# Kernel optimization log

Measured on AMD Instinct MI355X. Metric: run time of the kernel, lower is better.

Reference implementation:

```python
import jax, jax.numpy as jnp
import numpy as np

D_MODEL = 1024
NUM_HEAD = 16
HIDDEN = D_MODEL // NUM_HEAD  # 64, also d_att
T = float(np.sqrt(HIDDEN))
L = 2048
BS = 2


def setup_inputs() -> dict:
    key = jax.random.key(0)
    ks = jax.random.split(key, 6)
    s = 1.0 / np.sqrt(D_MODEL)
    return {
        "Q": jax.random.normal(ks[0], (L, BS, D_MODEL), jnp.float32),
        "K": jax.random.normal(ks[1], (L, BS, D_MODEL), jnp.float32),
        "V": jax.random.normal(ks[2], (L, BS, D_MODEL), jnp.float32),
        "WQ": jax.random.normal(ks[3], (D_MODEL, D_MODEL), jnp.float32) * s,
        "bQ": jnp.zeros((D_MODEL,), jnp.float32),
        "WK": jax.random.normal(ks[4], (D_MODEL, D_MODEL), jnp.float32) * s,
        "bK": jnp.zeros((D_MODEL,), jnp.float32),
        "Wp": jax.random.normal(ks[5], (D_MODEL, 2 * D_MODEL), jnp.float32) * s,
        "bp": jnp.zeros((D_MODEL,), jnp.float32),
    }


def reference(Q, K, V, WQ, bQ, WK, bK, Wp, bp):
    # inputs are sequence-first: [L, bs, d_model]
    Lq, bs, _ = Q.shape
    Qp = (Q @ WQ.T + bQ) / T
    Kp = K @ WK.T + bK
    # [L, bs, d_model] -> [bs, h, L, d]
    q = Qp.reshape(Lq, bs, NUM_HEAD, HIDDEN).transpose(1, 2, 0, 3)
    k = Kp.reshape(-1, bs, NUM_HEAD, HIDDEN).transpose(1, 2, 0, 3)
    v = V.reshape(-1, bs, NUM_HEAD, HIDDEN).transpose(1, 2, 0, 3)
    scores = jnp.einsum('bhqd,bhkd->bhqk', q, k)
    # use_dis: 2*QK - ||K||^2 per key
    scores = 2.0 * scores - jnp.sum(k * k, axis=-1)[:, :, None, :]
    attn = jax.nn.softmax(scores, axis=-1)
    out = jnp.einsum('bhqk,bhkd->bhqd', attn, v)
    out = out.transpose(2, 0, 1, 3).reshape(Lq, bs, D_MODEL)
    combined = jnp.concatenate([out, V], axis=-1)
    proj = combined @ Wp.T + bp
    return proj, attn
```

## Files before the change

### kernel.cpp

```cpp
#include <hip/hip_runtime.h>
#include <hip/hip_bf16.h>

#define L_SEQ 2048
#define BSZ 2
#define DMODEL 1024
#define NHEAD 16
#define NROWS 4096

typedef __attribute__((ext_vector_type(8))) short bf16x8;
typedef __attribute__((ext_vector_type(4))) float f32x4;
typedef unsigned short u16;
typedef unsigned int u32;

__device__ __forceinline__ u16 f2bf(float x) {
  union { __hip_bfloat16 h; u16 u; } cv;
  cv.h = __float2bfloat16(x);
  return cv.u;
}

__device__ __forceinline__ void async16(void* lds, const void* g) {
  __builtin_amdgcn_global_load_lds(
      (const __attribute__((address_space(1))) void*)g,
      (__attribute__((address_space(3))) void*)lds, 16, 0, 0);
}

__global__ __launch_bounds__(256) void cvt_kernel(const float* __restrict__ s,
                                                  u16* __restrict__ d, int n) {
  int i = (blockIdx.x * 256 + threadIdx.x) * 4;
  if (i >= n) return;
  float4 v = *(const float4*)(s + i);
  ushort4 o;
  o.x = f2bf(v.x); o.y = f2bf(v.y); o.z = f2bf(v.z); o.w = f2bf(v.w);
  *(ushort4*)(d + i) = o;
}

__global__ __launch_bounds__(256) void cvtV_kernel(const float* __restrict__ s,
                                                   u16* __restrict__ comb) {
  int i = (blockIdx.x * 256 + threadIdx.x) * 4;
  if (i >= NROWS * DMODEL) return;
  int r = i >> 10, c = i & 1023;
  float4 v = *(const float4*)(s + i);
  ushort4 o;
  o.x = f2bf(v.x); o.y = f2bf(v.y); o.z = f2bf(v.z); o.w = f2bf(v.w);
  *(ushort4*)(comb + (size_t)r * 2048 + 1024 + c) = o;
}

__global__ __launch_bounds__(256) void gemm_bt(
    const u16* __restrict__ A, const u16* __restrict__ B,
    const float* __restrict__ bias, float scale,
    u16* __restrict__ Cb, float* __restrict__ Cf, float* __restrict__ ksq_out,
    int M, int N, int K) {
  __shared__ u16 As[128 * 64];
  __shared__ u16 Bs[128 * 64];
  const int tid = threadIdx.x;
  const int w = tid >> 6, lane = tid & 63;
  const int quad = lane >> 4, m16 = lane & 15;
  const int wr = w >> 1, wc = w & 1;
  const int m0 = blockIdx.y * 128, n0 = blockIdx.x * 128;
  f32x4 acc[4][4] = {};

  for (int kt = 0; kt < K; kt += 64) {
    __syncthreads();
#pragma unroll
    for (int j = 0; j < 4; ++j) {
      int chunk = (w * 4 + j) * 64 + lane;
      int row = chunk >> 3, kc = chunk & 7;
      async16(As + (size_t)(w * 4 + j) * 512,
              A + (size_t)(m0 + row) * K + kt + kc * 8);
      async16(Bs + (size_t)(w * 4 + j) * 512,
              B + (size_t)(n0 + row) * K + kt + kc * 8);
    }
    __syncthreads();
#pragma unroll
    for (int kk = 0; kk < 2; ++kk) {
      bf16x8 af[4], bfr[4];
#pragma unroll
      for (int i = 0; i < 4; ++i)
        af[i] = *(const bf16x8*)(As + (wr * 64 + i * 16 + m16) * 64 + kk * 32 + quad * 8);
#pragma unroll
      for (int j = 0; j < 4; ++j)
        bfr[j] = *(const bf16x8*)(Bs + (wc * 64 + j * 16 + m16) * 64 + kk * 32 + quad * 8);
#pragma unroll
      for (int i = 0; i < 4; ++i)
#pragma unroll
        for (int j = 0; j < 4; ++j)
          acc[i][j] = __builtin_amdgcn_mfma_f32_16x16x32_bf16(af[i], bfr[j], acc[i][j], 0, 0, 0);
    }
  }

#pragma unroll
  for (int i = 0; i < 4; ++i) {
    int R0 = m0 + wr * 64 + i * 16 + quad * 4;
    float ksq_part[4] = {0.f, 0.f, 0.f, 0.f};
#pragma unroll
    for (int j = 0; j < 4; ++j) {
      int C = n0 + wc * 64 + j * 16 + m16;
      float bv = bias ? bias[C] : 0.0f;
#pragma unroll
      for (int r = 0; r < 4; ++r) {
        float v = (acc[i][j][r] + bv) * scale;
        size_t idx = (size_t)(R0 + r) * N + C;
        if (Cb) Cb[idx] = f2bf(v);
        if (Cf) Cf[idx] = v;
        if (ksq_out) ksq_part[r] += v * v;
      }
    }
    if (ksq_out) {
#pragma unroll
      for (int r = 0; r < 4; ++r) {
        float t = ksq_part[r];
        t += __shfl_xor(t, 1); t += __shfl_xor(t, 2);
        t += __shfl_xor(t, 4); t += __shfl_xor(t, 8);
        if (m16 == 0) {
          int R = R0 + r;
          int bb = R & 1, l = R >> 1;
          int h = (n0 + wc * 64) >> 6;
          ksq_out[(size_t)(bb * NHEAD + h) * L_SEQ + l] = t;
        }
      }
    }
  }
}

__global__ __launch_bounds__(256) void attn_kernel(
    const u16* __restrict__ qp, const u16* __restrict__ kp,
    const float* __restrict__ ksqg, const u16* __restrict__ comb_v,
    u16* __restrict__ comb_o, float* __restrict__ attn_out) {
  __shared__ u16 Qs[64 * 64];
  __shared__ u16 Ks[64 * 64];
  __shared__ u16 Vst[64 * 64];
  __shared__ u16 Ps[4 * 16 * 64];
  __shared__ float ksq_s[64];
  const int tid = threadIdx.x;
  const int w = tid >> 6, lane = tid & 63;
  const int quad = lane >> 4, m16 = lane & 15;
  const int qt = blockIdx.x, bh = blockIdx.y;
  const int b = bh >> 4, h = bh & 15;
  const int q0 = qt * 64;
  const int rsw = (m16 & 7) << 3;

#pragma unroll
  for (int j = 0; j < 2; ++j) {
    int chunk = (w * 2 + j) * 64 + lane;
    int row = chunk >> 3, kc = chunk & 7;
    int kcs = kc ^ (row & 7);
    async16(Qs + (size_t)(w * 2 + j) * 512,
            qp + (size_t)((q0 + row) * 2 + b) * 1024 + h * 64 + kcs * 8);
  }
  __syncthreads();
  bf16x8 aq0 = *(const bf16x8*)(Qs + (w * 16 + m16) * 64 + ((quad * 8) ^ rsw));
  bf16x8 aq1 = *(const bf16x8*)(Qs + (w * 16 + m16) * 64 + ((32 + quad * 8) ^ rsw));

  float lsum[4] = {0.f, 0.f, 0.f, 0.f};
  for (int kt = 0; kt < 32; ++kt) {
    __syncthreads();
#pragma unroll
    for (int j = 0; j < 2; ++j) {
      int chunk = (w * 2 + j) * 64 + lane;
      int row = chunk >> 3, kc = chunk & 7;
      int kcs = kc ^ (row & 7);
      async16(Ks + (size_t)(w * 2 + j) * 512,
              kp + (size_t)((kt * 64 + row) * 2 + b) * 1024 + h * 64 + kcs * 8);
    }
    if (tid < 64) ksq_s[tid] = ksqg[(size_t)bh * L_SEQ + kt * 64 + tid];
    __syncthreads();
#pragma unroll
    for (int j = 0; j < 4; ++j) {
      const u16* kr = Ks + (j * 16 + m16) * 64;
      bf16x8 bk0 = *(const bf16x8*)(kr + ((quad * 8) ^ rsw));
      bf16x8 bk1 = *(const bf16x8*)(kr + ((32 + quad * 8) ^ rsw));
      f32x4 s4 = {0.f, 0.f, 0.f, 0.f};
      __builtin_amdgcn_s_setprio(1);
      s4 = __builtin_amdgcn_mfma_f32_16x16x32_bf16(aq0, bk0, s4, 0, 0, 0);
      s4 = __builtin_amdgcn_mfma_f32_16x16x32_bf16(aq1, bk1, s4, 0, 0, 0);
      __builtin_amdgcn_s_setprio(0);
      float kq = ksq_s[j * 16 + m16];
#pragma unroll
      for (int r = 0; r < 4; ++r) lsum[r] += __expf(s4[r] - kq);
    }
  }
#pragma unroll
  for (int r = 0; r < 4; ++r) {
    float t = lsum[r];
    t += __shfl_xor(t, 1); t += __shfl_xor(t, 2);
    t += __shfl_xor(t, 4); t += __shfl_xor(t, 8);
    lsum[r] = 1.0f / t;
  }

  f32x4 o[4] = {};
  for (int kt = 0; kt < 32; ++kt) {
    __syncthreads();
#pragma unroll
    for (int j = 0; j < 2; ++j) {
      int chunk = (w * 2 + j) * 64 + lane;
      int row = chunk >> 3, kc = chunk & 7;
      int kcs = kc ^ (row & 7);
      async16(Ks + (size_t)(w * 2 + j) * 512,
              kp + (size_t)((kt * 64 + row) * 2 + b) * 1024 + h * 64 + kcs * 8);
    }
#pragma unroll
    for (int it = 0; it < 2; ++it) {
      int chunk = it * 256 + tid;
      int key = chunk >> 3, dc = chunk & 7;
      const u16* gp = comb_v + (size_t)((kt * 64 + key) * 2 + b) * 2048 + 1024 + h * 64 + dc * 8;
      uint4 u = *(const uint4*)gp;
      u32 parts[4] = {u.x, u.y, u.z, u.w};
#pragma unroll
      for (int q2 = 0; q2 < 4; ++q2) {
        int dA = dc * 8 + q2 * 2;
        int dB = dA + 1;
        int kxA = key ^ (((dc ^ (dA & 7)) & 7) << 3);
        int kxB = key ^ (((dc ^ (dB & 7)) & 7) << 3);
        Vst[dA * 64 + kxA] = (u16)(parts[q2] & 0xffffu);
        Vst[dB * 64 + kxB] = (u16)(parts[q2] >> 16);
      }
    }
    if (tid < 64) ksq_s[tid] = ksqg[(size_t)bh * L_SEQ + kt * 64 + tid];
    __syncthreads();
#pragma unroll
    for (int j = 0; j < 4; ++j) {
      const u16* kr = Ks + (j * 16 + m16) * 64;
      bf16x8 bk0 = *(const bf16x8*)(kr + ((quad * 8) ^ rsw));
      bf16x8 bk1 = *(const bf16x8*)(kr + ((32 + quad * 8) ^ rsw));
      f32x4 s4 = {0.f, 0.f, 0.f, 0.f};
      __builtin_amdgcn_s_setprio(1);
      s4 = __builtin_amdgcn_mfma_f32_16x16x32_bf16(aq0, bk0, s4, 0, 0, 0);
      s4 = __builtin_amdgcn_mfma_f32_16x16x32_bf16(aq1, bk1, s4, 0, 0, 0);
      __builtin_amdgcn_s_setprio(0);
      float kq = ksq_s[j * 16 + m16];
      size_t abase = ((size_t)bh * L_SEQ + q0 + w * 16 + quad * 4) * L_SEQ + kt * 64 + j * 16 + m16;
#pragma unroll
      for (int r = 0; r < 4; ++r) {
        float p = __expf(s4[r] - kq) * lsum[r];
        attn_out[abase + (size_t)r * L_SEQ] = p;
        int qrow = quad * 4 + r;
        int col = j * 16 + m16;
        Ps[w * 1024 + qrow * 64 + (col ^ ((qrow & 7) << 3))] = f2bf(p);
      }
    }
    __syncthreads();
#pragma unroll
    for (int kk = 0; kk < 2; ++kk) {
      bf16x8 pa = *(const bf16x8*)(Ps + w * 1024 + m16 * 64 +
                                   (((kk * 32 + quad * 8)) ^ rsw));
      __builtin_amdgcn_s_setprio(1);
#pragma unroll
      for (int j2 = 0; j2 < 4; ++j2) {
        int d = j2 * 16 + m16;
        int vx = (((d >> 3) ^ (d & 7)) & 7) << 3;
        bf16x8 bv = *(const bf16x8*)(Vst + d * 64 + ((kk * 32 + quad * 8) ^ vx));
        o[j2] = __builtin_amdgcn_mfma_f32_16x16x32_bf16(pa, bv, o[j2], 0, 0, 0);
      }
      __builtin_amdgcn_s_setprio(0);
    }
  }
#pragma unroll
  for (int j2 = 0; j2 < 4; ++j2) {
#pragma unroll
    for (int r = 0; r < 4; ++r) {
      int qrow = q0 + w * 16 + quad * 4 + r;
      comb_o[(size_t)(qrow * 2 + b) * 2048 + h * 64 + j2 * 16 + m16] = f2bf(o[j2][r]);
    }
  }
}

extern "C" void kernel_launch(void* const* d_in, const int* in_sizes, int n_in,
                              void* d_out, int out_size, void* d_ws, size_t ws_size,
                              hipStream_t stream) {
  const float* Q  = (const float*)d_in[0];
  const float* K  = (const float*)d_in[1];
  const float* V  = (const float*)d_in[2];
  const float* WQ = (const float*)d_in[3];
  const float* bQ = (const float*)d_in[4];
  const float* WK = (const float*)d_in[5];
  const float* bK = (const float*)d_in[6];
  const float* Wp = (const float*)d_in[7];
  const float* bp = (const float*)d_in[8];
  float* proj_out = (float*)d_out;
  float* attn_out = proj_out + (size_t)NROWS * DMODEL;

  char* ws = (char*)d_ws;
  const size_t MB = 1u << 20;
  u16* Qb   = (u16*)(ws + 0 * MB);
  u16* Kb   = (u16*)(ws + 8 * MB);
  u16* WQb  = (u16*)(ws + 16 * MB);
  u16* WKb  = (u16*)(ws + 18 * MB);
  u16* Wpb  = (u16*)(ws + 20 * MB);
  u16* qpb  = (u16*)(ws + 24 * MB);
  u16* kpb  = (u16*)(ws + 32 * MB);
  u16* comb = (u16*)(ws + 40 * MB);
  float* ksqb = (float*)(ws + 56 * MB);

  cvt_kernel<<<4096, 256, 0, stream>>>(Q, Qb, NROWS * DMODEL);
  cvt_kernel<<<4096, 256, 0, stream>>>(K, Kb, NROWS * DMODEL);
  cvt_kernel<<<1024, 256, 0, stream>>>(WQ, WQb, DMODEL * DMODEL);
  cvt_kernel<<<1024, 256, 0, stream>>>(WK, WKb, DMODEL * DMODEL);
  cvt_kernel<<<2048, 256, 0, stream>>>(Wp, Wpb, DMODEL * 2 * DMODEL);
  cvtV_kernel<<<4096, 256, 0, stream>>>(V, comb);

  gemm_bt<<<dim3(8, 32), 256, 0, stream>>>(Qb, WQb, bQ, 0.25f, qpb, nullptr, nullptr,
                                           NROWS, DMODEL, DMODEL);
  gemm_bt<<<dim3(8, 32), 256, 0, stream>>>(Kb, WKb, bK, 1.0f, kpb, nullptr, ksqb,
                                           NROWS, DMODEL, DMODEL);
  attn_kernel<<<dim3(32, 32), 256, 0, stream>>>(qpb, kpb, ksqb, comb, comb, attn_out);
  gemm_bt<<<dim3(8, 32), 256, 0, stream>>>(comb, Wpb, bp, 1.0f, nullptr, proj_out, nullptr,
                                           NROWS, DMODEL, 2 * DMODEL);
}
```

Measured before the change: 834.5 us.

## Double-buffer K/V tiles in attention with pre-transposed V and larger query tiles

Rewrites the attention kernel to process 128 queries per block with 32 rows per wave. K and V tiles are double-buffered in dynamic shared memory via async global-to-LDS loads, and the next tile's key norms are prefetched into registers. A new kernel pre-transposes V into a bf16 head-major layout, which removes the per-iteration scalar LDS transpose scatter. Blocks are remapped for locality and an occupancy hint is added. The cost is 80KB of LDS per block and an extra transpose kernel reusing the Qb buffer.

```diff
diff --git a/kernel.cpp b/kernel.cpp
--- a/kernel.cpp
+++ b/kernel.cpp
@@ -43,6 +43,32 @@
   ushort4 o;
   o.x = f2bf(v.x); o.y = f2bf(v.y); o.z = f2bf(v.z); o.w = f2bf(v.w);
   *(ushort4*)(comb + (size_t)r * 2048 + 1024 + c) = o;
+}
+
+__global__ __launch_bounds__(256) void transposeV_kernel(const float* __restrict__ V,
+                                                         u16* __restrict__ vt) {
+  __shared__ u16 T[64][80];
+  const int tid = threadIdx.x;
+  const int k0 = blockIdx.x * 64;
+  const int bh = blockIdx.y;
+  const int b = bh >> 4, h = bh & 15;
+#pragma unroll
+  for (int u = 0; u < 4; ++u) {
+    int key = u * 16 + (tid >> 4);
+    int d4 = (tid & 15) * 4;
+    float4 v = *(const float4*)(V + ((size_t)(k0 + key) * 2 + b) * 1024 + h * 64 + d4);
+    T[d4 + 0][key] = f2bf(v.x);
+    T[d4 + 1][key] = f2bf(v.y);
+    T[d4 + 2][key] = f2bf(v.z);
+    T[d4 + 3][key] = f2bf(v.w);
+  }
+  __syncthreads();
+  int d = tid >> 2, kq = (tid & 3) * 16;
+  uint4 lo = *(const uint4*)&T[d][kq];
+  uint4 hi = *(const uint4*)&T[d][kq + 8];
+  u16* dst = vt + ((size_t)bh * 64 + d) * 2048 + k0 + kq;
+  *(uint4*)dst = lo;
+  *(uint4*)(dst + 8) = hi;
 }
 
 __global__ __launch_bounds__(256) void gemm_bt(
@@ -122,146 +148,226 @@
   }
 }
 
-__global__ __launch_bounds__(256) void attn_kernel(
+__global__ __launch_bounds__(256, 2) void attn_kernel(
     const u16* __restrict__ qp, const u16* __restrict__ kp,
-    const float* __restrict__ ksqg, const u16* __restrict__ comb_v,
+    const float* __restrict__ ksqg, const u16* __restrict__ vt,
     u16* __restrict__ comb_o, float* __restrict__ attn_out) {
-  __shared__ u16 Qs[64 * 64];
-  __shared__ u16 Ks[64 * 64];
-  __shared__ u16 Vst[64 * 64];
-  __shared__ u16 Ps[4 * 16 * 64];
-  __shared__ float ksq_s[64];
+  extern __shared__ u16 smem[];
+
   const int tid = threadIdx.x;
   const int w = tid >> 6, lane = tid & 63;
   const int quad = lane >> 4, m16 = lane & 15;
-  const int qt = blockIdx.x, bh = blockIdx.y;
+  const int id = blockIdx.x;
+  const int wg = (id & 7) * 64 + (id >> 3);
+  const int bh = wg >> 4, qt = wg & 15;
   const int b = bh >> 4, h = bh & 15;
-  const int q0 = qt * 64;
-  const int rsw = (m16 & 7) << 3;
-
-#pragma unroll
-  for (int j = 0; j < 2; ++j) {
-    int chunk = (w * 2 + j) * 64 + lane;
-    int row = chunk >> 3, kc = chunk & 7;
-    int kcs = kc ^ (row & 7);
-    async16(Qs + (size_t)(w * 2 + j) * 512,
-            qp + (size_t)((q0 + row) * 2 + b) * 1024 + h * 64 + kcs * 8);
-  }
+  const int q0 = qt * 128;
+  u16* psw = smem + 32768 + w * 2048;
+
+#pragma unroll
+  for (int u = 0; u < 4; ++u) {
+    int base = u * 256 + w * 64;
+    int chunk = base + lane;
+    int kpr = chunk >> 4, g = chunk & 15;
+    int gs = g ^ (kpr & 15);
+    int qrow = q0 + kpr * 2 + (gs >> 3);
+    int dg = gs & 7;
+    async16(smem + 8192 + base * 8, qp + ((size_t)(qrow * 2 + b)) * 1024 + h * 64 + dg * 8);
+  }
+#pragma unroll
+  for (int u = 0; u < 4; ++u) {
+    int base = u * 256 + w * 64;
+    int chunk = base + lane;
+    int kpr = chunk >> 4, g = chunk & 15;
+    int gs = g ^ (kpr & 15);
+    int key = kpr * 2 + (gs >> 3);
+    int dg = gs & 7;
+    async16(smem + base * 8, kp + ((size_t)(key * 2 + b)) * 1024 + h * 64 + dg * 8);
+  }
+  float kqc[8], kqn[8];
+#pragma unroll
+  for (int j = 0; j < 8; ++j) kqc[j] = ksqg[(size_t)bh * L_SEQ + j * 16 + m16];
   __syncthreads();
-  bf16x8 aq0 = *(const bf16x8*)(Qs + (w * 16 + m16) * 64 + ((quad * 8) ^ rsw));
-  bf16x8 aq1 = *(const bf16x8*)(Qs + (w * 16 + m16) * 64 + ((32 + quad * 8) ^ rsw));
-
-  float lsum[4] = {0.f, 0.f, 0.f, 0.f};
-  for (int kt = 0; kt < 32; ++kt) {
+
+  bf16x8 aq[2][2];
+#pragma unroll
+  for (int qs = 0; qs < 2; ++qs)
+#pragma unroll
+    for (int hf = 0; hf < 2; ++hf) {
+      int rowloc = w * 32 + qs * 16 + m16;
+      int kpr = rowloc >> 1, hi2 = rowloc & 1;
+      int gs = hi2 * 8 + hf * 4 + quad;
+      int g = gs ^ (kpr & 15);
+      aq[qs][hf] = *(const bf16x8*)(smem + 8192 + kpr * 128 + g * 8);
+    }
+  __syncthreads();
+
+  float ls[2][4] = {};
+  for (int t = 0; t < 16; ++t) {
+    const int cur = t & 1;
+    const u16* kb = smem + (cur ? 8192 : 0);
+    u16* kbn = smem + (cur ? 0 : 8192);
+    if (t < 15) {
+#pragma unroll
+      for (int u = 0; u < 4; ++u) {
+        int base = u * 256 + w * 64;
+        int chunk = base + lane;
+        int kpr = chunk >> 4, g = chunk & 15;
+        int gs = g ^ (kpr & 15);
+        int key = (t + 1) * 128 + kpr * 2 + (gs >> 3);
+        int dg = gs & 7;
+        async16(kbn + base * 8, kp + ((size_t)(key * 2 + b)) * 1024 + h * 64 + dg * 8);
+      }
+#pragma unroll
+      for (int j = 0; j < 8; ++j)
+        kqn[j] = ksqg[(size_t)bh * L_SEQ + (t + 1) * 128 + j * 16 + m16];
+    }
+#pragma unroll
+    for (int j = 0; j < 8; ++j) {
+      int kpr = j * 8 + (m16 >> 1);
+      int hi2 = m16 & 1;
+      int g0 = (hi2 * 8 + quad) ^ (kpr & 15);
+      int g1 = (hi2 * 8 + 4 + quad) ^ (kpr & 15);
+      bf16x8 bk0 = *(const bf16x8*)(kb + kpr * 128 + g0 * 8);
+      bf16x8 bk1 = *(const bf16x8*)(kb + kpr * 128 + g1 * 8);
+      f32x4 s0 = {0.f, 0.f, 0.f, 0.f}, s1 = {0.f, 0.f, 0.f, 0.f};
+      __builtin_amdgcn_s_setprio(1);
+      s0 = __builtin_amdgcn_mfma_f32_16x16x32_bf16(aq[0][0], bk0, s0, 0, 0, 0);
+      s0 = __builtin_amdgcn_mfma_f32_16x16x32_bf16(aq[0][1], bk1, s0, 0, 0, 0);
+      s1 = __builtin_amdgcn_mfma_f32_16x16x32_bf16(aq[1][0], bk0, s1, 0, 0, 0);
+      s1 = __builtin_amdgcn_mfma_f32_16x16x32_bf16(aq[1][1], bk1, s1, 0, 0, 0);
+      __builtin_amdgcn_s_setprio(0);
+      float kq = kqc[j];
+#pragma unroll
+      for (int r = 0; r < 4; ++r) {
+        ls[0][r] += __expf(s0[r] - kq);
+        ls[1][r] += __expf(s1[r] - kq);
+      }
+    }
+    if (t < 15) {
+#pragma unroll
+      for (int j = 0; j < 8; ++j) kqc[j] = kqn[j];
+    }
     __syncthreads();
-#pragma unroll
-    for (int j = 0; j < 2; ++j) {
-      int chunk = (w * 2 + j) * 64 + lane;
-      int row = chunk >> 3, kc = chunk & 7;
-      int kcs = kc ^ (row & 7);
-      async16(Ks + (size_t)(w * 2 + j) * 512,
-              kp + (size_t)((kt * 64 + row) * 2 + b) * 1024 + h * 64 + kcs * 8);
-    }
-    if (tid < 64) ksq_s[tid] = ksqg[(size_t)bh * L_SEQ + kt * 64 + tid];
+  }
+  float linv[2][4];
+#pragma unroll
+  for (int qs = 0; qs < 2; ++qs)
+#pragma unroll
+    for (int r = 0; r < 4; ++r) {
+      float tt = ls[qs][r];
+      tt += __shfl_xor(tt, 1); tt += __shfl_xor(tt, 2);
+      tt += __shfl_xor(tt, 4); tt += __shfl_xor(tt, 8);
+      linv[qs][r] = 1.0f / tt;
+    }
+
+#pragma unroll
+  for (int u = 0; u < 4; ++u) {
+    int base = u * 256 + w * 64;
+    int chunk = base + lane;
+    int kpr = chunk >> 4, g = chunk & 15;
+    int gs = g ^ (kpr & 15);
+    int key = kpr * 2 + (gs >> 3);
+    int dg = gs & 7;
+    async16(smem + base * 8, kp + ((size_t)(key * 2 + b)) * 1024 + h * 64 + dg * 8);
+  }
+#pragma unroll
+  for (int u = 0; u < 4; ++u) {
+    int base = u * 256 + w * 64;
+    int chunk = base + lane;
+    int d = chunk >> 4, g = chunk & 15;
+    int gs = g ^ (d & 15);
+    async16(smem + 16384 + base * 8, vt + ((size_t)bh * 64 + d) * 2048 + gs * 8);
+  }
+#pragma unroll
+  for (int j = 0; j < 8; ++j) kqc[j] = ksqg[(size_t)bh * L_SEQ + j * 16 + m16];
+  __syncthreads();
+
+  f32x4 o[2][4] = {};
+  for (int t = 0; t < 16; ++t) {
+    const int cur = t & 1;
+    const u16* kb = smem + (cur ? 8192 : 0);
+    const u16* vb = smem + 16384 + (cur ? 8192 : 0);
+    u16* kbn = smem + (cur ? 0 : 8192);
+    u16* vbn = smem + 16384 + (cur ? 0 : 8192);
+    if (t < 15) {
+#pragma unroll
+      for (int u = 0; u < 4; ++u) {
+        int base = u * 256 + w * 64;
+        int chunk = base + lane;
+        int kpr = chunk >> 4, g = chunk & 15;
+        int gs = g ^ (kpr & 15);
+        int key = (t + 1) * 128 + kpr * 2 + (gs >> 3);
+        int dg = gs & 7;
+        async16(kbn + base * 8, kp + ((size_t)(key * 2 + b)) * 1024 + h * 64 + dg * 8);
+      }
+#pragma unroll
+      for (int u = 0; u < 4; ++u) {
+        int base = u * 256 + w * 64;
+        int chunk = base + lane;
+        int d = chunk >> 4, g = chunk & 15;
+        int gs = g ^ (d & 15);
+        async16(vbn + base * 8,
+                vt + ((size_t)bh * 64 + d) * 2048 + (t + 1) * 128 + gs * 8);
+      }
+#pragma unroll
+      for (int j = 0; j < 8; ++j)
+        kqn[j] = ksqg[(size_t)bh * L_SEQ + (t + 1) * 128 + j * 16 + m16];
+    }
+#pragma unroll
+    for (int qs = 0; qs < 2; ++qs) {
+#pragma unroll
+      for (int j = 0; j < 8; ++j) {
+        int kpr = j * 8 + (m16 >> 1);
+        int hi2 = m16 & 1;
+        int g0 = (hi2 * 8 + quad) ^ (kpr & 15);
+        int g1 = (hi2 * 8 + 4 + quad) ^ (kpr & 15);
+        bf16x8 bk0 = *(const bf16x8*)(kb + kpr * 128 + g0 * 8);
+        bf16x8 bk1 = *(const bf16x8*)(kb + kpr * 128 + g1 * 8);
+        f32x4 s = {0.f, 0.f, 0.f, 0.f};
+        s = __builtin_amdgcn_mfma_f32_16x16x32_bf16(aq[qs][0], bk0, s, 0, 0, 0);
+        s = __builtin_amdgcn_mfma_f32_16x16x32_bf16(aq[qs][1], bk1, s, 0, 0, 0);
+        float kq = kqc[j];
+        size_t abase = ((size_t)bh * L_SEQ + q0 + w * 32 + qs * 16 + quad * 4) * L_SEQ +
+                       t * 128 + j * 16 + m16;
+#pragma unroll
+        for (int r = 0; r < 4; ++r) {
+          float p = __expf(s[r] - kq) * linv[qs][r];
+          attn_out[abase + (size_t)r * L_SEQ] = p;
+          int row = quad * 4 + r;
+          int gw = (j * 2 + (m16 >> 3)) ^ row;
+          psw[row * 128 + gw * 8 + (m16 & 7)] = f2bf(p);
+        }
+      }
+      __builtin_amdgcn_s_setprio(1);
+#pragma unroll
+      for (int kk = 0; kk < 4; ++kk) {
+        bf16x8 pa = *(const bf16x8*)(psw + m16 * 128 + (((kk * 4 + quad) ^ m16)) * 8);
+#pragma unroll
+        for (int j2 = 0; j2 < 4; ++j2) {
+          int d = j2 * 16 + m16;
+          bf16x8 bv = *(const bf16x8*)(vb + d * 128 + (((kk * 4 + quad) ^ m16)) * 8);
+          o[qs][j2] = __builtin_amdgcn_mfma_f32_16x16x32_bf16(pa, bv, o[qs][j2], 0, 0, 0);
+        }
+      }
+      __builtin_amdgcn_s_setprio(0);
+    }
+    if (t < 15) {
+#pragma unroll
+      for (int j = 0; j < 8; ++j) kqc[j] = kqn[j];
+    }
     __syncthreads();
-#pragma unroll
-    for (int j = 0; j < 4; ++j) {
-      const u16* kr = Ks + (j * 16 + m16) * 64;
-      bf16x8 bk0 = *(const bf16x8*)(kr + ((quad * 8) ^ rsw));
-      bf16x8 bk1 = *(const bf16x8*)(kr + ((32 + quad * 8) ^ rsw));
-      f32x4 s4 = {0.f, 0.f, 0.f, 0.f};
-      __builtin_amdgcn_s_setprio(1);
-      s4 = __builtin_amdgcn_mfma_f32_16x16x32_bf16(aq0, bk0, s4, 0, 0, 0);
-      s4 = __builtin_amdgcn_mfma_f32_16x16x32_bf16(aq1, bk1, s4, 0, 0, 0);
-      __builtin_amdgcn_s_setprio(0);
-      float kq = ksq_s[j * 16 + m16];
-#pragma unroll
-      for (int r = 0; r < 4; ++r) lsum[r] += __expf(s4[r] - kq);
-    }
-  }
-#pragma unroll
-  for (int r = 0; r < 4; ++r) {
-    float t = lsum[r];
-    t += __shfl_xor(t, 1); t += __shfl_xor(t, 2);
-    t += __shfl_xor(t, 4); t += __shfl_xor(t, 8);
-    lsum[r] = 1.0f / t;
-  }
-
-  f32x4 o[4] = {};
-  for (int kt = 0; kt < 32; ++kt) {
-    __syncthreads();
-#pragma unroll
-    for (int j = 0; j < 2; ++j) {
-      int chunk = (w * 2 + j) * 64 + lane;
-      int row = chunk >> 3, kc = chunk & 7;
-      int kcs = kc ^ (row & 7);
-      async16(Ks + (size_t)(w * 2 + j) * 512,
-              kp + (size_t)((kt * 64 + row) * 2 + b) * 1024 + h * 64 + kcs * 8);
-    }
-#pragma unroll
-    for (int it = 0; it < 2; ++it) {
-      int chunk = it * 256 + tid;
-      int key = chunk >> 3, dc = chunk & 7;
-      const u16* gp = comb_v + (size_t)((kt * 64 + key) * 2 + b) * 2048 + 1024 + h * 64 + dc * 8;
-      uint4 u = *(const uint4*)gp;
-      u32 parts[4] = {u.x, u.y, u.z, u.w};
-#pragma unroll
-      for (int q2 = 0; q2 < 4; ++q2) {
-        int dA = dc * 8 + q2 * 2;
-        int dB = dA + 1;
-        int kxA = key ^ (((dc ^ (dA & 7)) & 7) << 3);
-        int kxB = key ^ (((dc ^ (dB & 7)) & 7) << 3);
-        Vst[dA * 64 + kxA] = (u16)(parts[q2] & 0xffffu);
-        Vst[dB * 64 + kxB] = (u16)(parts[q2] >> 16);
-      }
-    }
-    if (tid < 64) ksq_s[tid] = ksqg[(size_t)bh * L_SEQ + kt * 64 + tid];
-    __syncthreads();
-#pragma unroll
-    for (int j = 0; j < 4; ++j) {
-      const u16* kr = Ks + (j * 16 + m16) * 64;
-      bf16x8 bk0 = *(const bf16x8*)(kr + ((quad * 8) ^ rsw));
-      bf16x8 bk1 = *(const bf16x8*)(kr + ((32 + quad * 8) ^ rsw));
-      f32x4 s4 = {0.f, 0.f, 0.f, 0.f};
-      __builtin_amdgcn_s_setprio(1);
-      s4 = __builtin_amdgcn_mfma_f32_16x16x32_bf16(aq0, bk0, s4, 0, 0, 0);
-      s4 = __builtin_amdgcn_mfma_f32_16x16x32_bf16(aq1, bk1, s4, 0, 0, 0);
-      __builtin_amdgcn_s_setprio(0);
-      float kq = ksq_s[j * 16 + m16];
-      size_t abase = ((size_t)bh * L_SEQ + q0 + w * 16 + quad * 4) * L_SEQ + kt * 64 + j * 16 + m16;
+  }
+
+#pragma unroll
+  for (int qs = 0; qs < 2; ++qs)
+#pragma unroll
+    for (int j2 = 0; j2 < 4; ++j2)
 #pragma unroll
       for (int r = 0; r < 4; ++r) {
-        float p = __expf(s4[r] - kq) * lsum[r];
-        attn_out[abase + (size_t)r * L_SEQ] = p;
-        int qrow = quad * 4 + r;
-        int col = j * 16 + m16;
-        Ps[w * 1024 + qrow * 64 + (col ^ ((qrow & 7) << 3))] = f2bf(p);
-      }
-    }
-    __syncthreads();
-#pragma unroll
-    for (int kk = 0; kk < 2; ++kk) {
-      bf16x8 pa = *(const bf16x8*)(Ps + w * 1024 + m16 * 64 +
-                                   (((kk * 32 + quad * 8)) ^ rsw));
-      __builtin_amdgcn_s_setprio(1);
-#pragma unroll
-      for (int j2 = 0; j2 < 4; ++j2) {
-        int d = j2 * 16 + m16;
-        int vx = (((d >> 3) ^ (d & 7)) & 7) << 3;
-        bf16x8 bv = *(const bf16x8*)(Vst + d * 64 + ((kk * 32 + quad * 8) ^ vx));
-        o[j2] = __builtin_amdgcn_mfma_f32_16x16x32_bf16(pa, bv, o[j2], 0, 0, 0);
-      }
-      __builtin_amdgcn_s_setprio(0);
-    }
-  }
-#pragma unroll
-  for (int j2 = 0; j2 < 4; ++j2) {
-#pragma unroll
-    for (int r = 0; r < 4; ++r) {
-      int qrow = q0 + w * 16 + quad * 4 + r;
-      comb_o[(size_t)(qrow * 2 + b) * 2048 + h * 64 + j2 * 16 + m16] = f2bf(o[j2][r]);
-    }
-  }
+        int qrow = q0 + w * 32 + qs * 16 + quad * 4 + r;
+        comb_o[(size_t)(qrow * 2 + b) * 2048 + h * 64 + j2 * 16 + m16] = f2bf(o[qs][j2][r]);
+      }
 }
 
 extern "C" void kernel_launch(void* const* d_in, const int* in_sizes, int n_in,
@@ -290,6 +396,7 @@
   u16* kpb  = (u16*)(ws + 32 * MB);
   u16* comb = (u16*)(ws + 40 * MB);
   float* ksqb = (float*)(ws + 56 * MB);
+  u16* Vt = Qb;
 
   cvt_kernel<<<4096, 256, 0, stream>>>(Q, Qb, NROWS * DMODEL);
   cvt_kernel<<<4096, 256, 0, stream>>>(K, Kb, NROWS * DMODEL);
@@ -302,7 +409,11 @@
                                            NROWS, DMODEL, DMODEL);
   gemm_bt<<<dim3(8, 32), 256, 0, stream>>>(Kb, WKb, bK, 1.0f, kpb, nullptr, ksqb,
                                            NROWS, DMODEL, DMODEL);
-  attn_kernel<<<dim3(32, 32), 256, 0, stream>>>(qpb, kpb, ksqb, comb, comb, attn_out);
+  transposeV_kernel<<<dim3(32, 32), 256, 0, stream>>>(V, Vt);
+
+  (void)hipFuncSetAttribute(reinterpret_cast<const void*>(attn_kernel),
+                            hipFuncAttributeMaxDynamicSharedMemorySize, 81920);
+  attn_kernel<<<512, 256, 81920, stream>>>(qpb, kpb, ksqb, Vt, comb, attn_out);
   gemm_bt<<<dim3(8, 32), 256, 0, stream>>>(comb, Wpb, bp, 1.0f, nullptr, proj_out, nullptr,
                                            NROWS, DMODEL, 2 * DMODEL);
 }
```

Result: faster. 784.4 us (-6.0%).
